# Optimization experiments

Hardware: AMD Instinct MI355X
Metric: run time of the kernel (lower is better)

## Reference

```python
import jax, jax.numpy as jnp
from jax import lax
import numpy as np

B, T, H = 128, 512, 512  # batch, seq_length, hidden_dim (== input_dim)


def _xavier(key, shape):
    fan_in, fan_out = shape[1], shape[0]
    limit = float(np.sqrt(6.0 / (fan_in + fan_out)))
    return jax.random.uniform(key, shape, jnp.float32, -limit, limit)


def setup_inputs() -> dict:
    key = jax.random.key(0)
    ks = jax.random.split(key, 10)
    s = 1.0 / np.sqrt(H)  # torch LSTM default init range
    return {
        "x": jax.random.normal(ks[0], (B, T, H), jnp.float32),
        "W_ih": jax.random.uniform(ks[1], (4 * H, H), jnp.float32, -s, s),
        "W_hh": jax.random.uniform(ks[2], (4 * H, H), jnp.float32, -s, s),
        "b_ih": jax.random.uniform(ks[3], (4 * H,), jnp.float32, -s, s),
        "b_hh": jax.random.uniform(ks[4], (4 * H,), jnp.float32, -s, s),
        "Ve": _xavier(ks[5], (1, H)),
        "U1": _xavier(ks[6], (H, 2 * H)),
        "U2": _xavier(ks[7], (H, H)),
        "W_out": _xavier(ks[8], (2, H)),
        "b_out": jnp.zeros((2,), jnp.float32),
    }


def _lstm(x, W_ih, W_hh, b_ih, b_hh):
    # x: [B, T, D] -> hidden states [B, T, H]; PyTorch gate order i,f,g,o
    b = b_ih + b_hh
    # precompute input projections for all timesteps: [T, B, 4H]
    xg = jnp.einsum('btd,gd->tbg', x, W_ih) + b

    def step(carry, xt):
        h, c = carry
        g = xt + h @ W_hh.T  # [B, 4H]
        i, f, gg, o = jnp.split(g, 4, axis=1)
        c = jax.nn.sigmoid(f) * c + jax.nn.sigmoid(i) * jnp.tanh(gg)
        h = jax.nn.sigmoid(o) * jnp.tanh(c)
        return (h, c), h

    h0 = jnp.zeros((x.shape[0], W_hh.shape[1]), x.dtype)
    (_, _), hs = lax.scan(step, (h0, h0), xg)
    return jnp.swapaxes(hs, 0, 1)  # [B, T, H]


def reference(x, W_ih, W_hh, b_ih, b_hh, Ve, U1, U2, W_out, b_out):
    h = _lstm(x, W_ih, W_hh, b_ih, b_hh)  # [B, T, H]
    h_last = h[:, -1, :]  # [B, H]
    # additive attention, vectorized over all timesteps
    Hdim = h.shape[-1]
    u1 = jnp.einsum('bth,gh->btg', h, U1[:, :Hdim]) + jnp.einsum('bh,gh->bg', h_last, U1[:, Hdim:])[:, None, :]
    u2 = jnp.einsum('btd,gd->btg', x, U2)
    u = jnp.tanh(u1 + u2)  # [B, T, H]
    e = jnp.einsum('bth,h->bt', u, Ve[0])
    alpha = jax.nn.softmax(e, axis=1)  # [B, T]
    context = jnp.einsum('bt,bth->bh', alpha, h)  # [B, H]
    params = context @ W_out.T + b_out  # [B, 2]
    mu = params[:, 0]
    sigma = jax.nn.softplus(params[:, 1]) + 1e-5
    return (mu, sigma)
```

## Files before the change

kernel.cpp:

```cpp
#include <hip/hip_runtime.h>
#include <stdint.h>


using short8  = __attribute__((ext_vector_type(8))) short;
using short4v = __attribute__((ext_vector_type(4))) short;
using floatx4 = __attribute__((ext_vector_type(4))) float;

#define MFMA16(a, b, c) __builtin_amdgcn_mfma_f32_16x16x32_bf16((a), (b), (c), 0, 0, 0)

__device__ __forceinline__ unsigned short f2b(float f) {
    unsigned u = __float_as_uint(f);
    u += 0x7FFFu + ((u >> 16) & 1u);
    return (unsigned short)(u >> 16);
}
__device__ __forceinline__ float b2f(unsigned short h) {
    return __uint_as_float(((unsigned)h) << 16);
}
__device__ __forceinline__ float sigm(float x) { return 1.0f / (1.0f + __expf(-x)); }
__device__ __forceinline__ float tanh_(float x) { return 1.0f - 2.0f / (__expf(2.0f * x) + 1.0f); }

__global__ __launch_bounds__(256) void prep(
    const float* __restrict__ x, const float* __restrict__ Wih, const float* __restrict__ Whh,
    const float* __restrict__ bih, const float* __restrict__ bhh,
    const float* __restrict__ U1, const float* __restrict__ U2,
    unsigned short* __restrict__ x_bf, unsigned short* __restrict__ Wih_bf,
    unsigned short* __restrict__ Whh_bf, unsigned short* __restrict__ U1a,
    unsigned short* __restrict__ U1b, unsigned short* __restrict__ U2b,
    float* __restrict__ bias)
{
    const long long NX4 = 33554432LL / 4;
    const long long NREST = 1048576LL + 1048576LL + 524288LL + 262144LL + 2048LL;
    const long long total = NX4 + NREST;
    for (long long u = (long long)blockIdx.x * 256 + threadIdx.x; u < total;
         u += (long long)gridDim.x * 256) {
        if (u < NX4) {
            float4 v = ((const float4*)x)[u];
            short4v o;
            o[0] = (short)f2b(v.x); o[1] = (short)f2b(v.y);
            o[2] = (short)f2b(v.z); o[3] = (short)f2b(v.w);
            *(short4v*)&x_bf[u * 4] = o;
        } else {
            long long i = u - NX4;
            if (i < 1048576) { Wih_bf[i] = f2b(Wih[i]); continue; }
            i -= 1048576;
            if (i < 1048576) { Whh_bf[i] = f2b(Whh[i]); continue; }
            i -= 1048576;
            if (i < 524288) {
                int row = (int)(i >> 10), col = (int)(i & 1023);
                if (col < 512) U1a[row * 512 + col] = f2b(U1[i]);
                else           U1b[row * 512 + (col - 512)] = f2b(U1[i]);
                continue;
            }
            i -= 524288;
            if (i < 262144) { U2b[i] = f2b(U2[i]); continue; }
            i -= 262144;
            bias[i] = bih[i] + bhh[i];
        }
    }
}

__device__ __forceinline__ void gemm_core(
    const unsigned short* __restrict__ A, long long lda,
    const unsigned short* __restrict__ Bm, long long ldb,
    unsigned short* __restrict__ C, long long ldc,
    const float* __restrict__ bias, int mode,
    int m0, int n0, int tid, unsigned short* sbuf)
{
    unsigned short* At = sbuf;
    unsigned short* Bt = sbuf + 128 * 72;
    unsigned short* Ct = sbuf;

    const int wv = tid >> 6, lane = tid & 63, l15 = lane & 15, q = lane >> 4;
    const int wm = wv & 1, wn = wv >> 1;

    floatx4 acc[4][4];
    for (int i = 0; i < 4; i++)
        for (int j = 0; j < 4; j++) acc[i][j] = (floatx4){0.f, 0.f, 0.f, 0.f};

    for (int k0 = 0; k0 < 512; k0 += 64) {
        for (int p = 0; p < 4; p++) {
            int idx = tid + p * 256;
            int row = idx >> 3, ch = idx & 7;
            *(short8*)&At[row * 72 + ch * 8] =
                *(const short8*)&A[(long long)(m0 + row) * lda + k0 + ch * 8];
            *(short8*)&Bt[row * 72 + ch * 8] =
                *(const short8*)&Bm[(long long)(n0 + row) * ldb + k0 + ch * 8];
        }
        __syncthreads();
        for (int ks = 0; ks < 64; ks += 32) {
            short8 af[4], bfv[4];
            for (int mi = 0; mi < 4; mi++)
                af[mi] = *(const short8*)&At[(wm * 64 + mi * 16 + l15) * 72 + ks + q * 8];
            for (int ni = 0; ni < 4; ni++)
                bfv[ni] = *(const short8*)&Bt[(wn * 64 + ni * 16 + l15) * 72 + ks + q * 8];
            for (int mi = 0; mi < 4; mi++)
                for (int ni = 0; ni < 4; ni++)
                    acc[mi][ni] = MFMA16(af[mi], bfv[ni], acc[mi][ni]);
        }
        __syncthreads();
    }

    float bv[4];
    for (int ni = 0; ni < 4; ni++)
        bv[ni] = bias ? bias[n0 + wn * 64 + ni * 16 + l15] : 0.0f;

    for (int mi = 0; mi < 4; mi++)
        for (int ni = 0; ni < 4; ni++)
            for (int r = 0; r < 4; r++)
                Ct[(wm * 64 + mi * 16 + q * 4 + r) * 128 + wn * 64 + ni * 16 + l15] =
                    f2b(acc[mi][ni][r] + bv[ni]);
    __syncthreads();

    const int tt0 = m0 & 511, bglob = m0 >> 9;
    for (int p = 0; p < 8; p++) {
        int idx = tid + p * 256;
        int row = idx >> 4, ch = idx & 15;
        if (mode) {
            int n = n0 + ch * 8;
            int gate = n >> 9, jg = (n >> 4) & 31, c0 = gate * 16 + (n & 15);
            long long dst = (((long long)(tt0 + row) * 32 + jg) * 128 + bglob) * 64 + c0;
            *(short8*)&C[dst] = *(const short8*)&Ct[row * 128 + ch * 8];
        } else {
            *(short8*)&C[(long long)(m0 + row) * ldc + n0 + ch * 8] =
                *(const short8*)&Ct[row * 128 + ch * 8];
        }
    }
}

__global__ __launch_bounds__(256) void gemm_bt(
    const unsigned short* __restrict__ A, long long lda,
    const unsigned short* __restrict__ Bm, long long ldb,
    unsigned short* __restrict__ C, long long ldc,
    const float* __restrict__ bias, int mode, int mmul)
{
    __shared__ __align__(16) unsigned short sbuf[2 * 128 * 72];
    gemm_core(A, lda, Bm, ldb, C, ldc, bias, mode,
              blockIdx.x * mmul, blockIdx.y * 128, threadIdx.x, sbuf);
}

#define GEMM_WGS 6144
#define ATTN_WGS 2048
__global__ __launch_bounds__(256, 1) void mega(
    const unsigned short* __restrict__ xg,
    const unsigned short* __restrict__ Whh,
    unsigned short* __restrict__ h_all,
    unsigned int* __restrict__ ring,
    const unsigned short* __restrict__ x_bf,
    const unsigned short* __restrict__ Wih_bf,
    const float* __restrict__ bias,
    unsigned short* __restrict__ xg_out,
    int* __restrict__ syncp,
    const unsigned short* __restrict__ U1a,
    const unsigned short* __restrict__ U2b)
{
    __shared__ __align__(16) char smem[36864];

    const int tid = threadIdx.x;

    if (blockIdx.x >= 64 && blockIdx.x < 64 + GEMM_WGS) {
        int g = blockIdx.x - 64;
        int ti = 1 + (g >> 11);
        int r2 = g & 2047;
        int b = r2 & 127;
        int n = r2 >> 7;
        gemm_core(x_bf, 512, Wih_bf, 512, xg_out, 2048, bias, 1,
                  b * 512 + ti * 128, n * 128, tid, (unsigned short*)smem);
        __syncthreads();
        if (tid == 0)
            __hip_atomic_fetch_add(&syncp[ti - 1], 1, __ATOMIC_RELEASE,
                                   __HIP_MEMORY_SCOPE_AGENT);
        return;
    }

    if (blockIdx.x >= 64 + GEMM_WGS) {
        const int g = blockIdx.x - 64 - GEMM_WGS;
        const int tt = g >> 7;
        const int b  = g & 127;
        const int t0 = tt * 32;
        const int bg = b >> 4;

        if (tid < 8) {
            while (__hip_atomic_load(&syncp[8 + bg * 8 + tid], __ATOMIC_RELAXED,
                                     __HIP_MEMORY_SCOPE_AGENT) < t0 + 32)
                __builtin_amdgcn_s_sleep(8);
        }
        __syncthreads();

        unsigned short* Bt2 = (unsigned short*)smem;
        unsigned short* At2 = (unsigned short*)smem + 512 * 32;

        const int wv = tid >> 6, lane = tid & 63, l15 = lane & 15, q = lane >> 4;

        floatx4 acc[2][8];
        for (int mi = 0; mi < 2; mi++)
            for (int ni = 0; ni < 8; ni++) acc[mi][ni] = (floatx4){0.f, 0.f, 0.f, 0.f};

        for (int it = 0; it < 32; it++) {
            const int phase = it >> 4, kk = (it & 15) * 32;
            const unsigned short* Bsrc = phase ? U2b : U1a;
            __syncthreads();
            for (int idx = tid; idx < 2048; idx += 256) {
                int row = idx >> 2, ch = idx & 3;
                *(short8*)&Bt2[row * 32 + ch * 8] =
                    *(const short8*)&Bsrc[(long long)row * 512 + kk + ch * 8];
            }
            if (tid < 128) {
                int row = tid >> 2, ch = tid & 3;
                if (phase == 0) {
                    unsigned long long* p = (unsigned long long*)
                        &h_all[((long long)b * 512 + t0 + row) * 512 + kk + ch * 8];
                    unsigned long long lo = __hip_atomic_load(p, __ATOMIC_RELAXED,
                                                              __HIP_MEMORY_SCOPE_AGENT);
                    unsigned long long hi = __hip_atomic_load(p + 1, __ATOMIC_RELAXED,
                                                              __HIP_MEMORY_SCOPE_AGENT);
                    unsigned long long* d = (unsigned long long*)&At2[row * 40 + ch * 8];
                    d[0] = lo; d[1] = hi;
                } else {
                    *(short8*)&At2[row * 40 + ch * 8] =
                        *(const short8*)&x_bf[((long long)b * 512 + t0 + row) * 512 + kk + ch * 8];
                }
            }
            __syncthreads();
            short8 af0 = *(const short8*)&At2[(l15) * 40 + q * 8];
            short8 af1 = *(const short8*)&At2[(16 + l15) * 40 + q * 8];
            for (int ni = 0; ni < 8; ni++) {
                short8 bfv = *(const short8*)&Bt2[(wv * 128 + ni * 16 + l15) * 32 + q * 8];
                acc[0][ni] = MFMA16(af0, bfv, acc[0][ni]);
                acc[1][ni] = MFMA16(af1, bfv, acc[1][ni]);
            }
        }
        for (int mi = 0; mi < 2; mi++)
            for (int ni = 0; ni < 8; ni++) {
                const int n = wv * 128 + ni * 16 + l15;
                #pragma unroll
                for (int r = 0; r < 4; r++) {
                    const int t = t0 + mi * 16 + q * 4 + r;
                    float* slot = (float*)&xg_out[(((long long)t * 32 + (n >> 5)) * 128 + b) * 64];
                    slot[n & 31] = acc[mi][ni][r];
                }
            }
        return;
    }

    __builtin_amdgcn_s_setprio(1);

    unsigned int (*At)[16 * 264] = (unsigned int (*)[16 * 264])smem;

    const int wv = tid >> 6, lane = tid & 63, l15 = lane & 15, q = lane >> 4;
    const int bg = blockIdx.x >> 3, jgb = blockIdx.x & 7;
    const int b0 = bg * 16;
    const int jg32 = jgb * 4 + wv;
    const int hid = jg32 * 16 + l15;

    short8 Wreg[4][16];
    #pragma unroll
    for (int ct = 0; ct < 4; ct++)
        #pragma unroll
        for (int kk = 0; kk < 16; kk++)
            Wreg[ct][kk] = *(const short8*)
                &Whh[(long long)(ct * 512 + hid) * 512 + kk * 32 + q * 8];

    float cst[4] = {0.f, 0.f, 0.f, 0.f};

    for (int t = 0; t < 512; t++) {
        if (t == 128 || t == 256 || t == 384) {
            if (tid == 0) {
                const int gi = (t >> 7) - 1;
                while (__hip_atomic_load(&syncp[gi], __ATOMIC_ACQUIRE,
                                         __HIP_MEMORY_SCOPE_AGENT) < 2048)
                    __builtin_amdgcn_s_sleep(8);
            }
            __syncthreads();
        }

        unsigned long long w[16];
        const int sl = (t - 1) & 1;
        unsigned long long* rb = (unsigned long long*)
            (ring + sl * 65536 + b0 * 512);
        if (t > 0) {
            #pragma unroll
            for (int i = 0; i < 16; i++)
                w[i] = __hip_atomic_load(&rb[tid + i * 256], __ATOMIC_RELAXED,
                                         __HIP_MEMORY_SCOPE_AGENT);
        }

        const long long xbase = ((long long)(t * 32 + jg32) * 128 + b0) * 64;
        floatx4 acc[4];
        #pragma unroll
        for (int ct = 0; ct < 4; ct++)
            #pragma unroll
            for (int r = 0; r < 4; r++)
                acc[ct][r] = b2f(xg[xbase + (q * 4 + r) * 64 + ct * 16 + l15]);
        floatx4 acc2[4];
        #pragma unroll
        for (int ct = 0; ct < 4; ct++) acc2[ct] = (floatx4){0.f, 0.f, 0.f, 0.f};

        if (t > 0) {
            const unsigned want = (unsigned)(t - 1);
            while (true) {
                unsigned bad = 0;
                #pragma unroll
                for (int i = 0; i < 16; i++) {
                    unsigned lo = (unsigned)(w[i] >> 16) & 0xFFFFu;
                    unsigned hi = (unsigned)(w[i] >> 48);
                    bad |= (lo ^ want) | (hi ^ want);
                }
                if (!bad) break;
                #pragma unroll
                for (int i = 0; i < 16; i++) {
                    unsigned lo = (unsigned)(w[i] >> 16) & 0xFFFFu;
                    unsigned hi = (unsigned)(w[i] >> 48);
                    if ((lo ^ want) | (hi ^ want))
                        w[i] = __hip_atomic_load(&rb[tid + i * 256], __ATOMIC_RELAXED,
                                                 __HIP_MEMORY_SCOPE_AGENT);
                }
            }
            unsigned int* dst = &At[sl][0];
            #pragma unroll
            for (int i = 0; i < 16; i++) {
                int idx = tid + i * 256;
                int row = idx >> 8, k = idx & 255;
                dst[row * 264 + k] =
                    (unsigned)(w[i] & 0xFFFFu) | ((unsigned)(w[i] >> 32) << 16);
            }
            __syncthreads();
            const unsigned int* ap = &At[sl][l15 * 264 + q * 4];
            #pragma unroll
            for (int kk = 0; kk < 8; kk++) {
                short8 af  = *(const short8*)(ap + kk * 16);
                short8 af2 = *(const short8*)(ap + (kk + 8) * 16);
                acc[0] = MFMA16(af, Wreg[0][kk], acc[0]);
                acc[1] = MFMA16(af, Wreg[1][kk], acc[1]);
                acc[2] = MFMA16(af, Wreg[2][kk], acc[2]);
                acc[3] = MFMA16(af, Wreg[3][kk], acc[3]);
                acc2[0] = MFMA16(af2, Wreg[0][kk + 8], acc2[0]);
                acc2[1] = MFMA16(af2, Wreg[1][kk + 8], acc2[1]);
                acc2[2] = MFMA16(af2, Wreg[2][kk + 8], acc2[2]);
                acc2[3] = MFMA16(af2, Wreg[3][kk + 8], acc2[3]);
            }
        }
        unsigned short hbv[4];
        #pragma unroll
        for (int r = 0; r < 4; r++) {
            float ig = sigm(acc[0][r] + acc2[0][r]);
            float fg = sigm(acc[1][r] + acc2[1][r]);
            float gv = tanh_(acc[2][r] + acc2[2][r]);
            float og = sigm(acc[3][r] + acc2[3][r]);
            cst[r] = fg * cst[r] + ig * gv;
            hbv[r] = f2b(og * tanh_(cst[r]));
        }
        #pragma unroll
        for (int r = 0; r < 4; r++) {
            const int b = b0 + q * 4 + r;
            __hip_atomic_store(&ring[(t & 1) * 65536 + b * 512 + hid],
                               ((unsigned)t << 16) | hbv[r], __ATOMIC_RELAXED,
                               __HIP_MEMORY_SCOPE_AGENT);
        }
        #pragma unroll
        for (int r = 0; r < 4; r++) {
            const int b = b0 + q * 4 + r;
            int o = __shfl_xor((int)hbv[r], 1);
            if (!(l15 & 1)) {
                unsigned v = (unsigned)hbv[r] | (((unsigned)(unsigned short)o) << 16);
                __hip_atomic_store(
                    (unsigned*)&h_all[(long long)b * 262144 + (long long)t * 512 + hid],
                    v, __ATOMIC_RELAXED, __HIP_MEMORY_SCOPE_AGENT);
            }
        }
        if ((t & 15) == 15) {
            __syncthreads();
            if (tid == 0)
                __hip_atomic_store(&syncp[8 + (int)blockIdx.x], t + 1,
                                   __ATOMIC_RELAXED, __HIP_MEMORY_SCOPE_AGENT);
        }
    }
}

__global__ __launch_bounds__(256) void attn_out(
    const unsigned short* __restrict__ a_xg,
    const unsigned short* __restrict__ h_all,
    const unsigned short* __restrict__ u1bv,
    const float* __restrict__ Ve,
    const float* __restrict__ Wout, const float* __restrict__ bout,
    float* __restrict__ outp)
{
    __shared__ float se[512];
    __shared__ float sm[512];
    __shared__ float red[8];
    const int b = blockIdx.x, tid = threadIdx.x;
    const int wv = tid >> 6, lane = tid & 63;

    const int n0 = lane * 8;
    float ve[8], ub[8];
    #pragma unroll
    for (int j = 0; j < 8; j++) {
        ve[j] = Ve[n0 + j];
        ub[j] = b2f(u1bv[b * 512 + n0 + j]);
    }
    for (int it = 0; it < 64; it++) {
        const int t = it * 8 + wv * 2;
        const float* s0p = (const float*)
            &a_xg[(((long long)t * 32 + (n0 >> 5)) * 128 + b) * 64];
        const float* s1p = (const float*)
            &a_xg[(((long long)(t + 1) * 32 + (n0 >> 5)) * 128 + b) * 64];
        float4 a0 = *(const float4*)&s0p[n0 & 31];
        float4 a1 = *(const float4*)&s0p[(n0 & 31) + 4];
        float4 a2 = *(const float4*)&s1p[n0 & 31];
        float4 a3 = *(const float4*)&s1p[(n0 & 31) + 4];
        float s0 = ve[0] * tanh_(a0.x + ub[0]) + ve[1] * tanh_(a0.y + ub[1])
                 + ve[2] * tanh_(a0.z + ub[2]) + ve[3] * tanh_(a0.w + ub[3])
                 + ve[4] * tanh_(a1.x + ub[4]) + ve[5] * tanh_(a1.y + ub[5])
                 + ve[6] * tanh_(a1.z + ub[6]) + ve[7] * tanh_(a1.w + ub[7]);
        float s1 = ve[0] * tanh_(a2.x + ub[0]) + ve[1] * tanh_(a2.y + ub[1])
                 + ve[2] * tanh_(a2.z + ub[2]) + ve[3] * tanh_(a2.w + ub[3])
                 + ve[4] * tanh_(a3.x + ub[4]) + ve[5] * tanh_(a3.y + ub[5])
                 + ve[6] * tanh_(a3.z + ub[6]) + ve[7] * tanh_(a3.w + ub[7]);
        #pragma unroll
        for (int off = 1; off <= 32; off <<= 1) {
            s0 += __shfl_xor(s0, off);
            s1 += __shfl_xor(s1, off);
        }
        if (lane == 0) { se[t] = s0; se[t + 1] = s1; }
    }
    __syncthreads();

    float e0 = se[tid], e1 = se[256 + tid];
    float mx = fmaxf(e0, e1);
    for (int off = 32; off; off >>= 1) mx = fmaxf(mx, __shfl_xor(mx, off));
    if (lane == 0) red[wv] = mx;
    __syncthreads();
    mx = fmaxf(fmaxf(red[0], red[1]), fmaxf(red[2], red[3]));

    float s0 = __expf(e0 - mx), s1 = __expf(e1 - mx);
    sm[tid] = s0; sm[256 + tid] = s1;
    float ss = s0 + s1;
    for (int off = 32; off; off >>= 1) ss += __shfl_xor(ss, off);
    if (lane == 0) red[4 + wv] = ss;
    __syncthreads();
    float inv = 1.0f / (red[4] + red[5] + red[6] + red[7]);

    const unsigned int* hp = (const unsigned int*)(h_all + (long long)b * 262144);
    float a0 = 0.f, a1 = 0.f;
    for (int t = 0; t < 512; t += 4) {
        #pragma unroll
        for (int j = 0; j < 4; j++) {
            float al = sm[t + j];
            unsigned v = hp[(t + j) * 256 + tid];
            a0 += al * b2f((unsigned short)(v & 0xFFFFu));
            a1 += al * b2f((unsigned short)(v >> 16));
        }
    }
    a0 *= inv; a1 *= inv;

    float q0 = a0 * Wout[2 * tid] + a1 * Wout[2 * tid + 1];
    float q1 = a0 * Wout[512 + 2 * tid] + a1 * Wout[512 + 2 * tid + 1];
    for (int off = 32; off; off >>= 1) { q0 += __shfl_xor(q0, off); q1 += __shfl_xor(q1, off); }
    __syncthreads();
    if (lane == 0) { red[wv] = q0; red[4 + wv] = q1; }
    __syncthreads();
    if (tid == 0) {
        float P0 = red[0] + red[1] + red[2] + red[3] + bout[0];
        float P1 = red[4] + red[5] + red[6] + red[7] + bout[1];
        outp[b] = P0;
        float sp = (P1 > 15.0f) ? P1 : log1pf(__expf(P1));
        outp[128 + b] = sp + 1e-5f;
    }
}

extern "C" void kernel_launch(void* const* d_in, const int* in_sizes, int n_in,
                              void* d_out, int out_size, void* d_ws, size_t ws_size,
                              hipStream_t stream)
{
    const float* x    = (const float*)d_in[0];
    const float* Wih  = (const float*)d_in[1];
    const float* Whh  = (const float*)d_in[2];
    const float* bih  = (const float*)d_in[3];
    const float* bhh  = (const float*)d_in[4];
    const float* Ve   = (const float*)d_in[5];
    const float* U1   = (const float*)d_in[6];
    const float* U2   = (const float*)d_in[7];
    const float* Wout = (const float*)d_in[8];
    const float* bout = (const float*)d_in[9];
    float* out = (float*)d_out;

    char* ws = (char*)d_ws;
    size_t off = 0;
    auto alloc = [&](size_t bytes) -> void* {
        void* p = ws + off;
        off += (bytes + 255) & ~(size_t)255;
        return p;
    };
    unsigned short* x_bf   = (unsigned short*)alloc(33554432ull * 2);
    unsigned short* Wih_bf = (unsigned short*)alloc(1048576ull * 2);
    unsigned short* Whh_bf = (unsigned short*)alloc(1048576ull * 2);
    unsigned short* U1a    = (unsigned short*)alloc(262144ull * 2);
    unsigned short* U1b    = (unsigned short*)alloc(262144ull * 2);
    unsigned short* U2b    = (unsigned short*)alloc(262144ull * 2);
    float*          bias   = (float*)alloc(2048ull * 4);
    unsigned short* xg     = (unsigned short*)alloc(134217728ull * 2);
    unsigned short* h_all  = (unsigned short*)alloc(33554432ull * 2);
    unsigned short* u1bv   = (unsigned short*)alloc(65536ull * 2);
    unsigned int*   ring   = (unsigned int*)alloc(131072ull * 4);
    int*            syncp  = (int*)alloc(512ull);
    if (off > ws_size) return;

    hipMemsetAsync(syncp, 0, 512, stream);
    prep<<<4096, 256, 0, stream>>>(x, Wih, Whh, bih, bhh, U1, U2,
                                   x_bf, Wih_bf, Whh_bf, U1a, U1b, U2b, bias);
    gemm_bt<<<dim3(128, 16), 256, 0, stream>>>(x_bf, 512, Wih_bf, 512,
                                               xg, 2048, bias, 1, 512);
    mega<<<64 + GEMM_WGS + ATTN_WGS, 256, 0, stream>>>(
        xg, Whh_bf, h_all, ring, x_bf, Wih_bf, bias, xg, syncp, U1a, U2b);
    gemm_bt<<<dim3(1, 4), 256, 0, stream>>>(h_all + 511 * 512, 262144, U1b, 512,
                                            u1bv, 512, nullptr, 0, 128);
    attn_out<<<128, 256, 0, stream>>>(xg, h_all, u1bv, Ve, Wout, bout, out);
}
```

Baseline: 2.913 ms.

## Collapse GEMM sync counters, pad sync slots, enlarge LDS, and simplify the recurrent MFMA chain

The GEMM workgroups inside the mega kernel now signal a single counter, and the recurrent blocks wait on it once at t=128 instead of at three chunk boundaries. The GEMM tile order is also reordered so all time-chunks of a batch row are interleaved. Per-block progress counters are padded onto separate 64-byte lines to avoid false sharing. The shared buffer is enlarged to 86016 bytes (which limits co-residency to one workgroup per CU) and the attention B tile gets padded rows to cut bank conflicts. In the recurrent step, setprio is dropped, the xg load is moved ahead of the ring poll, and the two interleaved MFMA accumulator chains are merged into one 16-deep chain. The single chain lengthens the serial MFMA dependency on the critical recurrence, and waiting for all GEMM tiles at t=128 may stall the recurrence longer.

```diff
diff --git a/kernel.cpp b/kernel.cpp
--- a/kernel.cpp
+++ b/kernel.cpp
@@ -153,21 +153,21 @@
     const unsigned short* __restrict__ U1a,
     const unsigned short* __restrict__ U2b)
 {
-    __shared__ __align__(16) char smem[36864];
+    __shared__ __align__(16) char smem[86016];
 
     const int tid = threadIdx.x;
 
     if (blockIdx.x >= 64 && blockIdx.x < 64 + GEMM_WGS) {
         int g = blockIdx.x - 64;
-        int ti = 1 + (g >> 11);
-        int r2 = g & 2047;
-        int b = r2 & 127;
-        int n = r2 >> 7;
+        int b = g & 127;
+        int r = g >> 7;
+        int ti = 1 + (r % 3);
+        int n = r / 3;
         gemm_core(x_bf, 512, Wih_bf, 512, xg_out, 2048, bias, 1,
                   b * 512 + ti * 128, n * 128, tid, (unsigned short*)smem);
         __syncthreads();
         if (tid == 0)
-            __hip_atomic_fetch_add(&syncp[ti - 1], 1, __ATOMIC_RELEASE,
+            __hip_atomic_fetch_add(&syncp[0], 1, __ATOMIC_RELEASE,
                                    __HIP_MEMORY_SCOPE_AGENT);
         return;
     }
@@ -180,14 +180,15 @@
         const int bg = b >> 4;
 
         if (tid < 8) {
-            while (__hip_atomic_load(&syncp[8 + bg * 8 + tid], __ATOMIC_RELAXED,
+            while (__hip_atomic_load(&syncp[16 + (bg * 8 + tid) * 16],
+                                     __ATOMIC_RELAXED,
                                      __HIP_MEMORY_SCOPE_AGENT) < t0 + 32)
                 __builtin_amdgcn_s_sleep(8);
         }
         __syncthreads();
 
         unsigned short* Bt2 = (unsigned short*)smem;
-        unsigned short* At2 = (unsigned short*)smem + 512 * 32;
+        unsigned short* At2 = (unsigned short*)smem + 512 * 40;
 
         const int wv = tid >> 6, lane = tid & 63, l15 = lane & 15, q = lane >> 4;
 
@@ -201,7 +202,7 @@
             __syncthreads();
             for (int idx = tid; idx < 2048; idx += 256) {
                 int row = idx >> 2, ch = idx & 3;
-                *(short8*)&Bt2[row * 32 + ch * 8] =
+                *(short8*)&Bt2[row * 40 + ch * 8] =
                     *(const short8*)&Bsrc[(long long)row * 512 + kk + ch * 8];
             }
             if (tid < 128) {
@@ -224,7 +225,7 @@
             short8 af0 = *(const short8*)&At2[(l15) * 40 + q * 8];
             short8 af1 = *(const short8*)&At2[(16 + l15) * 40 + q * 8];
             for (int ni = 0; ni < 8; ni++) {
-                short8 bfv = *(const short8*)&Bt2[(wv * 128 + ni * 16 + l15) * 32 + q * 8];
+                short8 bfv = *(const short8*)&Bt2[(wv * 128 + ni * 16 + l15) * 40 + q * 8];
                 acc[0][ni] = MFMA16(af0, bfv, acc[0][ni]);
                 acc[1][ni] = MFMA16(af1, bfv, acc[1][ni]);
             }
@@ -242,8 +243,6 @@
         return;
     }
 
-    __builtin_amdgcn_s_setprio(1);
-
     unsigned int (*At)[16 * 264] = (unsigned int (*)[16 * 264])smem;
 
     const int wv = tid >> 6, lane = tid & 63, l15 = lane & 15, q = lane >> 4;
@@ -263,40 +262,32 @@
     float cst[4] = {0.f, 0.f, 0.f, 0.f};
 
     for (int t = 0; t < 512; t++) {
-        if (t == 128 || t == 256 || t == 384) {
+        if (t == 128) {
             if (tid == 0) {
-                const int gi = (t >> 7) - 1;
-                while (__hip_atomic_load(&syncp[gi], __ATOMIC_ACQUIRE,
-                                         __HIP_MEMORY_SCOPE_AGENT) < 2048)
+                while (__hip_atomic_load(&syncp[0], __ATOMIC_ACQUIRE,
+                                         __HIP_MEMORY_SCOPE_AGENT) < GEMM_WGS)
                     __builtin_amdgcn_s_sleep(8);
             }
             __syncthreads();
         }
-
-        unsigned long long w[16];
-        const int sl = (t - 1) & 1;
-        unsigned long long* rb = (unsigned long long*)
-            (ring + sl * 65536 + b0 * 512);
+        const long long xbase = ((long long)(t * 32 + jg32) * 128 + b0) * 64;
+        floatx4 acc[4];
+        #pragma unroll
+        for (int ct = 0; ct < 4; ct++)
+            #pragma unroll
+            for (int r = 0; r < 4; r++)
+                acc[ct][r] = b2f(xg[xbase + (q * 4 + r) * 64 + ct * 16 + l15]);
+
         if (t > 0) {
+            const unsigned want = (unsigned)(t - 1);
+            const int sl = (t - 1) & 1;
+            unsigned long long* rb = (unsigned long long*)
+                (ring + sl * 65536 + b0 * 512);
+            unsigned long long w[16];
             #pragma unroll
             for (int i = 0; i < 16; i++)
                 w[i] = __hip_atomic_load(&rb[tid + i * 256], __ATOMIC_RELAXED,
                                          __HIP_MEMORY_SCOPE_AGENT);
-        }
-
-        const long long xbase = ((long long)(t * 32 + jg32) * 128 + b0) * 64;
-        floatx4 acc[4];
-        #pragma unroll
-        for (int ct = 0; ct < 4; ct++)
-            #pragma unroll
-            for (int r = 0; r < 4; r++)
-                acc[ct][r] = b2f(xg[xbase + (q * 4 + r) * 64 + ct * 16 + l15]);
-        floatx4 acc2[4];
-        #pragma unroll
-        for (int ct = 0; ct < 4; ct++) acc2[ct] = (floatx4){0.f, 0.f, 0.f, 0.f};
-
-        if (t > 0) {
-            const unsigned want = (unsigned)(t - 1);
             while (true) {
                 unsigned bad = 0;
                 #pragma unroll
@@ -326,26 +317,21 @@
             __syncthreads();
             const unsigned int* ap = &At[sl][l15 * 264 + q * 4];
             #pragma unroll
-            for (int kk = 0; kk < 8; kk++) {
-                short8 af  = *(const short8*)(ap + kk * 16);
-                short8 af2 = *(const short8*)(ap + (kk + 8) * 16);
+            for (int kk = 0; kk < 16; kk++) {
+                short8 af = *(const short8*)(ap + kk * 16);
                 acc[0] = MFMA16(af, Wreg[0][kk], acc[0]);
                 acc[1] = MFMA16(af, Wreg[1][kk], acc[1]);
                 acc[2] = MFMA16(af, Wreg[2][kk], acc[2]);
                 acc[3] = MFMA16(af, Wreg[3][kk], acc[3]);
-                acc2[0] = MFMA16(af2, Wreg[0][kk + 8], acc2[0]);
-                acc2[1] = MFMA16(af2, Wreg[1][kk + 8], acc2[1]);
-                acc2[2] = MFMA16(af2, Wreg[2][kk + 8], acc2[2]);
-                acc2[3] = MFMA16(af2, Wreg[3][kk + 8], acc2[3]);
             }
         }
         unsigned short hbv[4];
         #pragma unroll
         for (int r = 0; r < 4; r++) {
-            float ig = sigm(acc[0][r] + acc2[0][r]);
-            float fg = sigm(acc[1][r] + acc2[1][r]);
-            float gv = tanh_(acc[2][r] + acc2[2][r]);
-            float og = sigm(acc[3][r] + acc2[3][r]);
+            float ig = sigm(acc[0][r]);
+            float fg = sigm(acc[1][r]);
+            float gv = tanh_(acc[2][r]);
+            float og = sigm(acc[3][r]);
             cst[r] = fg * cst[r] + ig * gv;
             hbv[r] = f2b(og * tanh_(cst[r]));
         }
@@ -370,7 +356,7 @@
         if ((t & 15) == 15) {
             __syncthreads();
             if (tid == 0)
-                __hip_atomic_store(&syncp[8 + (int)blockIdx.x], t + 1,
+                __hip_atomic_store(&syncp[16 + (int)blockIdx.x * 16], t + 1,
                                    __ATOMIC_RELAXED, __HIP_MEMORY_SCOPE_AGENT);
         }
     }
@@ -501,10 +487,10 @@
     unsigned short* h_all  = (unsigned short*)alloc(33554432ull * 2);
     unsigned short* u1bv   = (unsigned short*)alloc(65536ull * 2);
     unsigned int*   ring   = (unsigned int*)alloc(131072ull * 4);
-    int*            syncp  = (int*)alloc(512ull);
+    int*            syncp  = (int*)alloc(8192ull);
     if (off > ws_size) return;
 
-    hipMemsetAsync(syncp, 0, 512, stream);
+    hipMemsetAsync(syncp, 0, 8192, stream);
     prep<<<4096, 256, 0, stream>>>(x, Wih, Whh, bih, bhh, U1, U2,
                                    x_bf, Wih_bf, Whh_bf, U1a, U1b, U2b, bias);
     gemm_bt<<<dim3(128, 16), 256, 0, stream>>>(x_bf, 512, Wih_bf, 512,
```

Result: faster. 2.562 ms (-12.1%).
